# Performance work log

Hardware: AMD Instinct MI355X
Metric: run time of the kernel (lower is better)

Reference implementation:

```python
import jax, jax.numpy as jnp
import numpy as np

D = 1024
H = 16
HD = D // H
LN_EPS = 1e-5
RMS_EPS = 1e-6


def layernorm(x, g, b):
    mu = jnp.mean(x, axis=-1, keepdims=True)
    var = jnp.mean(jnp.square(x - mu), axis=-1, keepdims=True)
    return (x - mu) * jax.lax.rsqrt(var + LN_EPS) * g + b


def rmsnorm(x, w):
    ms = jnp.mean(jnp.square(x), axis=-1, keepdims=True)
    return x * jax.lax.rsqrt(ms + RMS_EPS) * w


def setup_inputs() -> dict:
    key = jax.random.key(0)
    ks = jax.random.split(key, 8)
    s = 0.02
    ones = jnp.ones((D,), jnp.float32)
    zeros = jnp.zeros((D,), jnp.float32)
    return {
        "query_tokens": jax.random.normal(ks[0], (4, 512, D), jnp.float32),
        "point_features": jax.random.normal(ks[1], (4, 4096, D), jnp.float32),
        "ln_q_g": ones, "ln_q_b": zeros,
        "ln_kv_g": ones, "ln_kv_b": zeros,
        "Wq": jax.random.normal(ks[2], (D, D), jnp.float32) * s, "bq": zeros,
        "Wk": jax.random.normal(ks[3], (D, D), jnp.float32) * s, "bk": zeros,
        "Wv": jax.random.normal(ks[4], (D, D), jnp.float32) * s, "bv": zeros,
        "rms_q_w": ones, "rms_k_w": ones,
        "Wo": jax.random.normal(ks[5], (D, D), jnp.float32) * s, "bo": zeros,
        "ln_mlp_g": ones, "ln_mlp_b": zeros,
        "W1": jax.random.normal(ks[6], (D, 4 * D), jnp.float32) * s,
        "b1": jnp.zeros((4 * D,), jnp.float32),
        "W2": jax.random.normal(ks[7], (4 * D, D), jnp.float32) * s,
        "b2": zeros,
    }


def reference(query_tokens, point_features, ln_q_g, ln_q_b, ln_kv_g, ln_kv_b,
              Wq, bq, Wk, bk, Wv, bv, rms_q_w, rms_k_w, Wo, bo,
              ln_mlp_g, ln_mlp_b, W1, b1, W2, b2):
    B, K, _ = query_tokens.shape
    N = point_features.shape[1]
    q_in = layernorm(query_tokens, ln_q_g, ln_q_b)
    kv_in = layernorm(point_features, ln_kv_g, ln_kv_b)
    q = rmsnorm(q_in @ Wq + bq, rms_q_w)          # [B,K,D]
    k = rmsnorm(kv_in @ Wk + bk, rms_k_w)         # [B,N,D]
    v = kv_in @ Wv + bv                            # [B,N,D]
    q = q.reshape(B, K, H, HD)
    k = k.reshape(B, N, H, HD)
    v = v.reshape(B, N, H, HD)
    scores = jnp.einsum('bkhd,bnhd->bhkn', q, k) / jnp.sqrt(jnp.float32(HD))
    attn = jax.nn.softmax(scores, axis=-1)
    ctx = jnp.einsum('bhkn,bnhd->bkhd', attn, v).reshape(B, K, D)
    out = ctx @ Wo + bo + query_tokens
    h = layernorm(out, ln_mlp_g, ln_mlp_b)
    mlp = jax.nn.gelu(h @ W1 + b1, approximate=False) @ W2 + b2
    return out + mlp
```

## Files before the change

kernel.cpp:

```cpp
#include <hip/hip_runtime.h>
#include <math.h>

#define DD   1024
#define NHD  16
#define HDIM 64
#define BB   4
#define QN   512
#define KVN  4096
#define FF   4096

typedef __attribute__((ext_vector_type(8))) short bf16x8;
typedef __attribute__((ext_vector_type(4))) float f32x4;

__device__ __forceinline__ float b2f(ushort u){
  union { unsigned u32; float f; } x; x.u32 = ((unsigned)u)<<16; return x.f;
}
__device__ __forceinline__ ushort f2b(float f){
  unsigned u = __float_as_uint(f);
  unsigned r = (u + 0x7FFFu + ((u>>16)&1u)) >> 16;
  return (ushort)r;
}
__device__ __forceinline__ float ldx(const void* p, size_t i, int isbf){
  return isbf ? b2f(((const ushort*)p)[i]) : ((const float*)p)[i];
}
__device__ __forceinline__ int detect_bf(const void* gref){
  return ((const unsigned*)gref)[0] == 0x3F803F80u;
}

#if defined(__has_builtin)
#if __has_builtin(__builtin_amdgcn_global_load_lds)
#define HAS_GLL 1
#endif
#endif
#ifndef HAS_GLL
#define HAS_GLL 0
#endif
__device__ __forceinline__ void stage16(const ushort* g, ushort* lds_base, int lane){
#if HAS_GLL
  __builtin_amdgcn_global_load_lds(g, lds_base, 16, 0, 0);
#else
  *(uint4*)(lds_base + lane*8) = *(const uint4*)g;
#endif
}

__device__ __forceinline__ void wave_barrier(){
  asm volatile("" ::: "memory");
  __builtin_amdgcn_s_barrier();
  asm volatile("" ::: "memory");
}

__global__ __launch_bounds__(256)
void trans_all(const void* __restrict__ Wq, const void* __restrict__ Wk,
               const void* __restrict__ Wv, const void* __restrict__ Wo,
               const void* __restrict__ W1, const void* __restrict__ W2,
               ushort* __restrict__ WqT, ushort* __restrict__ WkvT,
               ushort* __restrict__ WoT,
               ushort* __restrict__ W1T, ushort* __restrict__ W2T,
               const void* __restrict__ gref)
{
  const int isbf = detect_bf(gref);
  int bid = blockIdx.x;
  const void* src; ushort* dst; int R, C, tid;
  if (bid < 1024){
    int s = bid >> 8; tid = bid & 255; R = 1024; C = 1024;
    src = (s==0) ? Wq : (s==1) ? Wk : (s==2) ? Wv : Wo;
    dst = (s==0) ? WqT : (s==1) ? WkvT : (s==2) ? (WkvT + (size_t)1024*1024) : WoT;
  } else if (bid < 2048){ tid = bid - 1024; src = W1; dst = W1T; R = 1024; C = 4096; }
  else                  { tid = bid - 2048; src = W2; dst = W2T; R = 4096; C = 1024; }
  int ntx = C >> 6;
  int tx = tid % ntx, ty = tid / ntx;
  int r0 = ty*64, c0 = tx*64;

  __shared__ __align__(16) ushort tile[64][72];
  int t = threadIdx.x;
  if (isbf){
    #pragma unroll
    for (int i=0;i<2;i++){
      int idx = t + i*256;
      int r = idx>>3, ch = idx&7;
      #pragma unroll
      for (int j=0;j<8;j++)
        tile[r][ch*8+j] = ((const ushort*)src)[(size_t)(r0+r)*C + c0 + ch*8 + j];
    }
  } else {
    #pragma unroll
    for (int i=0;i<2;i++){
      int idx = t + i*256;
      int r = idx>>3, ch = idx&7;
      const float* s4 = (const float*)src + (size_t)(r0+r)*C + c0 + ch*8;
      float4 f0 = *(const float4*)s4;
      float4 f1 = *(const float4*)(s4+4);
      tile[r][ch*8+0]=f2b(f0.x); tile[r][ch*8+1]=f2b(f0.y);
      tile[r][ch*8+2]=f2b(f0.z); tile[r][ch*8+3]=f2b(f0.w);
      tile[r][ch*8+4]=f2b(f1.x); tile[r][ch*8+5]=f2b(f1.y);
      tile[r][ch*8+6]=f2b(f1.z); tile[r][ch*8+7]=f2b(f1.w);
    }
  }
  __syncthreads();
  #pragma unroll
  for (int i=0;i<2;i++){
    int idx = t + i*256;
    int c = idx>>3, ch = idx&7;
    __align__(16) ushort tmp[8];
    #pragma unroll
    for (int j=0;j<8;j++) tmp[j] = tile[ch*8+j][c];
    *(uint4*)(dst + (size_t)(c0+c)*R + r0 + ch*8) = *(uint4*)tmp;
  }
}

__global__ __launch_bounds__(256)
void ln_all(const void* __restrict__ qtok, const void* __restrict__ pfeat,
            const void* __restrict__ gq, const void* __restrict__ bq,
            const void* __restrict__ gkv, const void* __restrict__ bkv,
            ushort* __restrict__ q_ln, ushort* __restrict__ kv_ln,
            const void* __restrict__ gref)
{
  const int isbf = detect_bf(gref);
  int row = blockIdx.x, t = threadIdx.x;
  const void* src; const void* g; const void* bb; ushort* dst; int r;
  if (row < BB*QN){ src = qtok;  g = gq;  bb = bq;  dst = q_ln;  r = row; }
  else            { src = pfeat; g = gkv; bb = bkv; dst = kv_ln; r = row - BB*QN; }
  int c0 = t*4;
  float v[4];
  if (isbf){
    #pragma unroll
    for (int i=0;i<4;i++) v[i] = b2f(((const ushort*)src)[(size_t)r*DD + c0 + i]);
  } else {
    float4 f = *(const float4*)((const float*)src + (size_t)r*DD + c0);
    v[0]=f.x; v[1]=f.y; v[2]=f.z; v[3]=f.w;
  }
  float s1=0.f, s2=0.f;
  #pragma unroll
  for (int i=0;i<4;i++){ s1 += v[i]; s2 += v[i]*v[i]; }
  #pragma unroll
  for (int off=32; off; off>>=1){ s1 += __shfl_xor(s1,off,64); s2 += __shfl_xor(s2,off,64); }
  __shared__ float r1[4], r2[4];
  int wave = t>>6;
  if ((t&63)==0){ r1[wave]=s1; r2[wave]=s2; }
  __syncthreads();
  s1 = r1[0]+r1[1]+r1[2]+r1[3];
  s2 = r2[0]+r2[1]+r2[2]+r2[3];
  float mu  = s1 * (1.0f/DD);
  float var = s2 * (1.0f/DD) - mu*mu;
  float rs  = rsqrtf(var + 1e-5f);
  union { ushort u[4]; uint2 w; } pk;
  #pragma unroll
  for (int i=0;i<4;i++)
    pk.u[i] = f2b((v[i]-mu)*rs*ldx(g,c0+i,isbf) + ldx(bb,c0+i,isbf));
  *(uint2*)(dst + (size_t)r*DD + c0) = pk.w;
}

__global__ __launch_bounds__(256)
void ln_combine(const float* __restrict__ p0, const float* __restrict__ p1,
                const void* __restrict__ bo, const void* __restrict__ qtok,
                const void* __restrict__ g, const void* __restrict__ bb,
                float* __restrict__ outb, ushort* __restrict__ y,
                const void* __restrict__ gref)
{
  const int isbf = detect_bf(gref);
  int row = blockIdx.x, t = threadIdx.x;
  int c0 = t*4;
  size_t base = (size_t)row*DD + c0;
  float4 a0 = *(const float4*)(p0 + base);
  float4 a1 = *(const float4*)(p1 + base);
  float v[4] = {a0.x+a1.x, a0.y+a1.y, a0.z+a1.z, a0.w+a1.w};
  if (isbf){
    #pragma unroll
    for (int i=0;i<4;i++)
      v[i] += b2f(((const ushort*)qtok)[base+i]) + b2f(((const ushort*)bo)[c0+i]);
  } else {
    float4 q4 = *(const float4*)((const float*)qtok + base);
    v[0] += q4.x + ((const float*)bo)[c0+0];
    v[1] += q4.y + ((const float*)bo)[c0+1];
    v[2] += q4.z + ((const float*)bo)[c0+2];
    v[3] += q4.w + ((const float*)bo)[c0+3];
  }
  float4 ov; ov.x=v[0]; ov.y=v[1]; ov.z=v[2]; ov.w=v[3];
  *(float4*)(outb + base) = ov;

  float s1=0.f, s2=0.f;
  #pragma unroll
  for (int i=0;i<4;i++){ s1 += v[i]; s2 += v[i]*v[i]; }
  #pragma unroll
  for (int off=32; off; off>>=1){ s1 += __shfl_xor(s1,off,64); s2 += __shfl_xor(s2,off,64); }
  __shared__ float r1[4], r2[4];
  int wave = t>>6;
  if ((t&63)==0){ r1[wave]=s1; r2[wave]=s2; }
  __syncthreads();
  s1 = r1[0]+r1[1]+r1[2]+r1[3];
  s2 = r2[0]+r2[1]+r2[2]+r2[3];
  float mu  = s1 * (1.0f/DD);
  float var = s2 * (1.0f/DD) - mu*mu;
  float rs  = rsqrtf(var + 1e-5f);
  union { ushort u[4]; uint2 w; } pk;
  #pragma unroll
  for (int i=0;i<4;i++)
    pk.u[i] = f2b((v[i]-mu)*rs*ldx(g,c0+i,isbf) + ldx(bb,c0+i,isbf));
  *(uint2*)(y + base) = pk.w;
}

__global__ __launch_bounds__(256)
void combine_w2(const float* __restrict__ parts, const void* __restrict__ b2,
                const float* __restrict__ res, void* __restrict__ out,
                const void* __restrict__ gref)
{
  const int isbf = detect_bf(gref);
  size_t i = ((size_t)blockIdx.x*256 + threadIdx.x)*4;
  float4 v = *(const float4*)(parts + i);
  #pragma unroll
  for (int z=1; z<4; z++){
    float4 p = *(const float4*)(parts + (size_t)z*BB*QN*DD + i);
    v.x+=p.x; v.y+=p.y; v.z+=p.z; v.w+=p.w;
  }
  float4 r = *(const float4*)(res + i);
  int col = (int)(i & (DD-1));
  v.x += r.x + ldx(b2,col+0,isbf);
  v.y += r.y + ldx(b2,col+1,isbf);
  v.z += r.z + ldx(b2,col+2,isbf);
  v.w += r.w + ldx(b2,col+3,isbf);
  if (isbf){
    union { ushort u[4]; uint2 w; } pk;
    pk.u[0]=f2b(v.x); pk.u[1]=f2b(v.y); pk.u[2]=f2b(v.z); pk.u[3]=f2b(v.w);
    *(uint2*)((ushort*)out + i) = pk.w;
  } else {
    *(float4*)((float*)out + i) = v;
  }
}

__global__ __launch_bounds__(256)
void rms_all(ushort* __restrict__ qb, const void* __restrict__ wq,
             ushort* __restrict__ kb, const void* __restrict__ wk,
             const void* __restrict__ gref)
{
  const int isbf = detect_bf(gref);
  int row = blockIdx.x, t = threadIdx.x;
  ushort* x; const void* w; int r;
  if (row < BB*QN){ x = qb; w = wq; r = row; }
  else            { x = kb; w = wk; r = row - BB*QN; }
  int c0 = t*4;
  union { ushort u[4]; uint2 w; } in;
  in.w = *(const uint2*)(x + (size_t)r*DD + c0);
  float v[4];
  #pragma unroll
  for (int i=0;i<4;i++) v[i] = b2f(in.u[i]);
  float s2 = 0.f;
  #pragma unroll
  for (int i=0;i<4;i++) s2 += v[i]*v[i];
  #pragma unroll
  for (int off=32; off; off>>=1) s2 += __shfl_xor(s2,off,64);
  __shared__ float r2[4];
  int wave = t>>6;
  if ((t&63)==0) r2[wave]=s2;
  __syncthreads();
  s2 = r2[0]+r2[1]+r2[2]+r2[3];
  float rs = rsqrtf(s2*(1.0f/DD) + 1e-6f);
  union { ushort u[4]; uint2 w; } pk;
  #pragma unroll
  for (int i=0;i<4;i++) pk.u[i] = f2b(v[i]*rs*ldx(w,c0+i,isbf));
  *(uint2*)(x + (size_t)r*DD + c0) = pk.w;
}

template<int ACT_GELU, int OUT_MODE, int RES_MODE>
__global__ __launch_bounds__(256)
void gemm_bt(const ushort* __restrict__ A, const ushort* __restrict__ BT,
             const void* __restrict__ bias,
             const void* __restrict__ res_ext, const float* __restrict__ res_f,
             void* __restrict__ Cout, void* __restrict__ Cout2,
             int M, int N, int Kdim, int Kstride,
             const void* __restrict__ gref)
{
  const int isbf = detect_bf(gref);
  __shared__ __align__(16) ushort As[128*64];
  __shared__ __align__(16) ushort Bs[128*64];
  const int bm = blockIdx.y * 128;
  const int bn = blockIdx.x * 128;
  const int kz = blockIdx.z;
  const int t = threadIdx.x;
  const int wave = t>>6, lane = t&63, quad = lane>>4, l16 = lane&15;
  const int wm = (wave&1)*64, wn = (wave>>1)*64;

  const ushort* ga[4]; const ushort* gb[4];
  #pragma unroll
  for (int j=0;j<4;j++){
    int row = (t>>3) + j*32;
    int g = ((t&7) - row) & 7;
    ga[j] = A  + (size_t)(bm+row)*Kstride + kz*Kdim + g*8;
    gb[j] = BT + (size_t)(bn+row)*Kstride + kz*Kdim + g*8;
  }

  int offA[2][4], offB[2][4];
  #pragma unroll
  for (int kk=0;kk<2;kk++)
    #pragma unroll
    for (int i=0;i<4;i++){
      int ra = wm + i*16 + l16;
      offA[kk][i] = ra*64 + ((quad + kk*4 + ra)&7)*8;
      int rb = wn + i*16 + l16;
      offB[kk][i] = rb*64 + ((quad + kk*4 + rb)&7)*8;
    }

  f32x4 zero = {0.f,0.f,0.f,0.f};
  f32x4 acc[4][4];
  #pragma unroll
  for (int i=0;i<4;i++)
    #pragma unroll
    for (int j=0;j<4;j++) acc[i][j] = zero;

  const int kiters = Kdim >> 6;
  for (int ki = 0; ki < kiters; ki++) {
    #pragma unroll
    for (int j=0;j<4;j++){
      stage16(ga[j], As + (size_t)(j*256 + wave*64)*8, lane);
      stage16(gb[j], Bs + (size_t)(j*256 + wave*64)*8, lane);
      ga[j] += 64; gb[j] += 64;
    }
    __syncthreads();
    #pragma unroll
    for (int kk=0;kk<2;kk++){
      bf16x8 af[4], bfr[4];
      #pragma unroll
      for (int i=0;i<4;i++){
        af[i]  = *(const bf16x8*)(As + offA[kk][i]);
        bfr[i] = *(const bf16x8*)(Bs + offB[kk][i]);
      }
      #pragma unroll
      for (int mt=0;mt<4;mt++)
        #pragma unroll
        for (int nt=0;nt<4;nt++)
          acc[mt][nt] = __builtin_amdgcn_mfma_f32_16x16x32_bf16(af[mt], bfr[nt], acc[mt][nt], 0,0,0);
    }
    __syncthreads();
  }

  if (OUT_MODE == 4){
    float* P = (float*)Cout + (size_t)kz*M*N;
    #pragma unroll
    for (int mt=0;mt<4;mt++){
      #pragma unroll
      for (int r=0;r<4;r++){
        int row = bm + wm + mt*16 + quad*4 + r;
        #pragma unroll
        for (int nt=0;nt<4;nt++){
          int col = bn + wn + nt*16 + l16;
          P[(size_t)row*N + col] = acc[mt][nt][r];
        }
      }
    }
    return;
  }

  if (OUT_MODE == 3){
    if (bn < 1024){
      float bv[4];
      #pragma unroll
      for (int nt=0;nt<4;nt++) bv[nt] = ldx(bias, bn + wn + nt*16 + l16, isbf);
      ushort* kout = (ushort*)Cout;
      #pragma unroll
      for (int mt=0;mt<4;mt++){
        #pragma unroll
        for (int r=0;r<4;r++){
          int row = bm + wm + mt*16 + quad*4 + r;
          #pragma unroll
          for (int nt=0;nt<4;nt++){
            int col = bn + wn + nt*16 + l16;
            kout[(size_t)row*1024 + col] = f2b(acc[mt][nt][r] + bv[nt]);
          }
        }
      }
    } else {
      float bv[4];
      #pragma unroll
      for (int nt=0;nt<4;nt++) bv[nt] = ldx(res_ext, bn-1024 + wn + nt*16 + l16, isbf);
      ushort* Vt = (ushort*)Cout2;
      #pragma unroll
      for (int mt=0;mt<4;mt++){
        int row0 = bm + wm + mt*16 + quad*4;
        int b = row0 >> 12, tok = row0 & (KVN-1);
        #pragma unroll
        for (int nt=0;nt<4;nt++){
          int cl = bn-1024 + wn + nt*16 + l16;
          union { ushort u[4]; uint2 w; } pk;
          #pragma unroll
          for (int r=0;r<4;r++) pk.u[r] = f2b(acc[mt][nt][r] + bv[nt]);
          size_t o = ((size_t)((b*NHD + (cl>>6))*HDIM + (cl&63)))*KVN + tok;
          *(uint2*)(Vt + o) = pk.w;
        }
      }
    }
    return;
  }

  float bv[4];
  #pragma unroll
  for (int nt=0;nt<4;nt++) bv[nt] = ldx(bias, bn + wn + nt*16 + l16, isbf);
  #pragma unroll
  for (int mt=0;mt<4;mt++){
    #pragma unroll
    for (int r=0;r<4;r++){
      int row = bm + wm + mt*16 + quad*4 + r;
      #pragma unroll
      for (int nt=0;nt<4;nt++){
        int col = bn + wn + nt*16 + l16;
        float v = acc[mt][nt][r] + bv[nt];
        if (ACT_GELU) v = 0.5f*v*(1.0f + erff(v*0.70710678118f));
        size_t oi = (size_t)row*N + col;
        if (RES_MODE==1) v += ldx(res_ext, oi, isbf);
        if (RES_MODE==2) v += res_f[oi];
        if (OUT_MODE==0)      ((ushort*)Cout)[oi] = f2b(v);
        else if (OUT_MODE==1) ((float*)Cout)[oi]  = v;
        else { if (isbf) ((ushort*)Cout)[oi] = f2b(v); else ((float*)Cout)[oi] = v; }
      }
    }
  }
}

#define G_HB  32768
#define G_RA0 0
#define G_RA1 8192
#define G_RB0 16384
#define G_RB1 24576

#define G_STAGE(src, R, tile) do{ \
  ushort* _d = ldsb + (((tile)&1)*G_HB + (R) + wave*1024); \
  stage16(src[0] + ((tile)<<6), _d,       lane); \
  stage16(src[1] + ((tile)<<6), _d + 512, lane); \
}while(0)

#define G_LDA(dst, base) \
  _Pragma("unroll") for (int kk=0;kk<2;kk++) \
  _Pragma("unroll") for (int m=0;m<4;m++) \
    dst[kk][m] = *(const bf16x8*)((base) + offA[kk][m]);

#define G_LDB(dst, base) \
  _Pragma("unroll") for (int kk=0;kk<2;kk++) \
  _Pragma("unroll") for (int n=0;n<2;n++) \
    dst[kk][n] = *(const bf16x8*)((base) + offB[kk][n]);

#define G_MM16(ar, br, MO, NO) \
  _Pragma("unroll") for (int kk=0;kk<2;kk++) \
  _Pragma("unroll") for (int m=0;m<4;m++) \
  _Pragma("unroll") for (int n=0;n<2;n++) \
    acc[m+(MO)][n+(NO)] = __builtin_amdgcn_mfma_f32_16x16x32_bf16(ar[kk][m], br[kk][n], acc[m+(MO)][n+(NO)], 0,0,0);

#define G_SYNC() do{ wave_barrier(); \
  asm volatile("s_waitcnt lgkmcnt(0)" ::: "memory"); \
  __builtin_amdgcn_sched_barrier(0); \
  __builtin_amdgcn_s_setprio(1); }while(0)

#define G_END() do{ __builtin_amdgcn_s_setprio(0); wave_barrier(); }while(0)

__global__ __launch_bounds__(512, 2)
void gemm256_kv(const ushort* __restrict__ A, const ushort* __restrict__ BT,
                const void* __restrict__ biasK, const void* __restrict__ biasV,
                ushort* __restrict__ Kout, ushort* __restrict__ Vt,
                int Kdim, const void* __restrict__ gref)
{
  const int isbf = detect_bf(gref);
  __shared__ __align__(16) ushort ldsb[65536];
  const int bm = blockIdx.y * 256;
  const int bn = blockIdx.x * 256;
  const int t = threadIdx.x;
  const int wave = t>>6, lane = t&63, quad = lane>>4, l16 = lane&15;
  const int wg = wave>>2, wn = wave&3;

  const ushort *sA0[2], *sA1[2], *sB0[2], *sB1[2];
  #pragma unroll
  for (int jj=0;jj<2;jj++){
    int r = (wave*2 + jj)*8 + (lane>>3);
    int g = ((lane&7) - r) & 7;
    int grA0 = r + (r & 64);
    int gc0  = (r & 31) + ((r >> 5) << 6);
    sA0[jj] = A  + (size_t)(bm + grA0     )*Kdim + g*8;
    sA1[jj] = A  + (size_t)(bm + grA0 + 64)*Kdim + g*8;
    sB0[jj] = BT + (size_t)(bn + gc0      )*Kdim + g*8;
    sB1[jj] = BT + (size_t)(bn + gc0 + 32 )*Kdim + g*8;
  }

  int offA[2][4], offB[2][2];
  #pragma unroll
  for (int kk=0;kk<2;kk++){
    int slot = ((kk*4 + quad + l16) & 7) * 8;
    #pragma unroll
    for (int m=0;m<4;m++) offA[kk][m] = (wg*64 + m*16 + l16)*64 + slot;
    #pragma unroll
    for (int n=0;n<2;n++) offB[kk][n] = (wn*32 + n*16 + l16)*64 + slot;
  }

  f32x4 zero = {0.f,0.f,0.f,0.f};
  f32x4 acc[8][4];
  #pragma unroll
  for (int i=0;i<8;i++)
    #pragma unroll
    for (int j=0;j<4;j++) acc[i][j] = zero;

  G_STAGE(sA0, G_RA0, 0);
  G_STAGE(sB0, G_RB0, 0);
  G_STAGE(sB1, G_RB1, 0);
  G_STAGE(sA1, G_RA1, 0);
  G_STAGE(sA0, G_RA0, 1);
  G_STAGE(sB1, G_RB1, 1);
  G_STAGE(sA1, G_RA1, 1);
  asm volatile("s_waitcnt vmcnt(6)" ::: "memory");
  wave_barrier();

  const int niter = Kdim >> 7;
  const ushort* L0 = ldsb;
  const ushort* L1 = ldsb + G_HB;
  bf16x8 a[2][4], b[2][2], b1[2][2];

  for (int i = 0; i < niter; ++i) {
    const bool st = (i + 1 < niter);
    G_LDA(a, L0 + G_RA0); G_LDB(b, L0 + G_RB0);
    G_STAGE(sB0, G_RB0, 2*i+1);
    G_SYNC(); G_MM16(a, b, 0, 0); G_END();
    G_LDB(b1, L0 + G_RB1);
    if (st) G_STAGE(sA0, G_RA0, 2*i+2);
    G_SYNC(); G_MM16(a, b1, 0, 2); G_END();
    G_LDA(a, L0 + G_RA1);
    if (st) G_STAGE(sB1, G_RB1, 2*i+2);
    G_SYNC(); G_MM16(a, b1, 4, 2); G_END();
    if (st) G_STAGE(sA1, G_RA1, 2*i+2);
    G_SYNC(); G_MM16(a, b, 4, 0);
    __builtin_amdgcn_s_setprio(0);
    if (st) { asm volatile("s_waitcnt vmcnt(6)" ::: "memory"); }
    else    { asm volatile("s_waitcnt vmcnt(0)" ::: "memory"); }
    wave_barrier();
    G_LDA(a, L1 + G_RA0); G_LDB(b, L1 + G_RB0);
    if (st) G_STAGE(sB0, G_RB0, 2*i+2);
    G_SYNC(); G_MM16(a, b, 0, 0); G_END();
    G_LDB(b1, L1 + G_RB1);
    if (st) G_STAGE(sA0, G_RA0, 2*i+3);
    G_SYNC(); G_MM16(a, b1, 0, 2); G_END();
    G_LDA(a, L1 + G_RA1);
    if (st) G_STAGE(sB1, G_RB1, 2*i+3);
    G_SYNC(); G_MM16(a, b1, 4, 2); G_END();
    if (st) G_STAGE(sA1, G_RA1, 2*i+3);
    G_SYNC(); G_MM16(a, b, 4, 0);
    __builtin_amdgcn_s_setprio(0);
    if (st) { asm volatile("s_waitcnt vmcnt(6)" ::: "memory"); }
    wave_barrier();
  }

  if (bn < 1024){
    float bvv[4];
    #pragma unroll
    for (int nt=0;nt<4;nt++) bvv[nt] = ldx(biasK, bn + wn*64 + nt*16 + l16, isbf);
    #pragma unroll
    for (int mt=0;mt<8;mt++){
      #pragma unroll
      for (int r=0;r<4;r++){
        int row = bm + wg*128 + mt*16 + quad*4 + r;
        #pragma unroll
        for (int nt=0;nt<4;nt++){
          int col = bn + wn*64 + nt*16 + l16;
          Kout[(size_t)row*1024 + col] = f2b(acc[mt][nt][r] + bvv[nt]);
        }
      }
    }
  } else {
    float bvv[4];
    #pragma unroll
    for (int nt=0;nt<4;nt++) bvv[nt] = ldx(biasV, bn - 1024 + wn*64 + nt*16 + l16, isbf);
    #pragma unroll
    for (int mt=0;mt<8;mt++){
      int row0 = bm + wg*128 + mt*16 + quad*4;
      int bi = row0 >> 12, tok = row0 & (KVN-1);
      #pragma unroll
      for (int nt=0;nt<4;nt++){
        int cl = bn - 1024 + wn*64 + nt*16 + l16;
        union { ushort u[4]; uint2 w2; } pk;
        #pragma unroll
        for (int r=0;r<4;r++) pk.u[r] = f2b(acc[mt][nt][r] + bvv[nt]);
        size_t o = ((size_t)((bi*NHD + (cl>>6))*HDIM + (cl&63)))*KVN + tok;
        *(uint2*)(Vt + o) = pk.w2;
      }
    }
  }
}

__global__ __launch_bounds__(256, 3)
void flash_attn3(const ushort* __restrict__ Q, const ushort* __restrict__ K,
                 const ushort* __restrict__ Vt, float* __restrict__ Op,
                 float* __restrict__ ML)
{
  __shared__ __align__(16) ushort Ks[128*72];
  __shared__ __align__(16) ushort Vs[64*136];
  __shared__ __align__(16) ushort Ps[4][16*136];
  const int bh = blockIdx.x, qt = blockIdx.y, hf = blockIdx.z;
  const int b = bh>>4, h = bh&15;
  const int t = threadIdx.x, wave = t>>6, lane = t&63, quad = lane>>4, l16 = lane&15;
  ushort* Pz = Ps[wave];

  const float QS = 0.125f * 1.4426950408889634f;
  bf16x8 qf[2][2];
  #pragma unroll
  for (int mt=0;mt<2;mt++){
    const ushort* qb = Q + (size_t)(b*QN + qt*128 + wave*32 + mt*16 + l16)*DD + h*HDIM;
    bf16x8 r0 = *(const bf16x8*)(qb + quad*8);
    bf16x8 r1 = *(const bf16x8*)(qb + 32 + quad*8);
    #pragma unroll
    for (int j=0;j<8;j++){
      qf[mt][0][j] = (short)f2b(b2f((ushort)r0[j]) * QS);
      qf[mt][1][j] = (short)f2b(b2f((ushort)r1[j]) * QS);
    }
  }

  f32x4 zero = {0.f,0.f,0.f,0.f};
  f32x4 o[2][4];
  #pragma unroll
  for (int mt=0;mt<2;mt++)
    #pragma unroll
    for (int nt=0;nt<4;nt++) o[mt][nt] = zero;
  float lp[2][4] = {{0.f,0.f,0.f,0.f},{0.f,0.f,0.f,0.f}};

  const ushort* kgb = K  + (size_t)(b*KVN + hf*1024)*DD + h*HDIM;
  const ushort* vtb = Vt + ((size_t)bh*HDIM)*KVN + hf*1024;
  const int kcs = t&7;

  for (int kv0 = 0; kv0 < 1024; kv0 += 128) {
    #pragma unroll
    for (int j=0;j<4;j++){
      int kr = (t>>3) + j*32;
      *(uint4*)(Ks + kr*72 + kcs*8) =
        *(const uint4*)(kgb + (size_t)(kv0+kr)*DD + kcs*8);
    }
    #pragma unroll
    for (int j=0;j<4;j++){
      int p = t + j*256; int vr = p>>4, vc = p&15;
      uint4 d = *(const uint4*)(vtb + (size_t)vr*KVN + kv0 + vc*8);
      ushort* pv = (ushort*)&d;
      ushort* vbp = Vs + vr*136 + (vc&1)*64 + (vc>>1);
      #pragma unroll
      for (int jj=0;jj<8;jj++) vbp[jj*8] = pv[jj];
    }
    __syncthreads();

    f32x4 pb[2][8];
    #pragma unroll
    for (int nt=0;nt<8;nt++){
      const ushort* kb = Ks + (nt*16+l16)*72 + quad*8;
      bf16x8 kf0 = *(const bf16x8*)kb;
      bf16x8 kf1 = *(const bf16x8*)(kb + 32);
      #pragma unroll
      for (int mt=0;mt<2;mt++){
        f32x4 a = __builtin_amdgcn_mfma_f32_16x16x32_bf16(qf[mt][0], kf0, zero, 0,0,0);
        a = __builtin_amdgcn_mfma_f32_16x16x32_bf16(qf[mt][1], kf1, a, 0,0,0);
        #pragma unroll
        for (int r=0;r<4;r++) a[r] = __builtin_amdgcn_exp2f(fminf(a[r], 88.f));
        pb[mt][nt] = a;
      }
    }
    #pragma unroll
    for (int mt=0;mt<2;mt++){
      #pragma unroll
      for (int r=0;r<4;r++){
        float ls = 0.f;
        bf16x8 pk;
        #pragma unroll
        for (int nt=0;nt<8;nt++){
          ls += pb[mt][nt][r];
          pk[nt] = (short)(__float_as_uint(pb[mt][nt][r]) >> 16);
        }
        lp[mt][r] += ls;
        *(bf16x8*)(Pz + (quad*4+r)*136 + l16*8) = pk;
      }
      #pragma unroll
      for (int kc=0;kc<4;kc++){
        bf16x8 pa = *(const bf16x8*)(Pz + l16*136 + kc*32 + quad*8);
        pb[mt][kc] = *(f32x4*)&pa;
      }
    }
    #pragma unroll
    for (int nt=0;nt<4;nt++){
      const ushort* vbr = Vs + (nt*16+l16)*136;
      #pragma unroll
      for (int kc=0;kc<4;kc++){
        bf16x8 vf = *(const bf16x8*)(vbr + kc*32 + quad*8);
        o[0][nt] = __builtin_amdgcn_mfma_f32_16x16x32_bf16(*(bf16x8*)&pb[0][kc], vf, o[0][nt], 0,0,0);
        o[1][nt] = __builtin_amdgcn_mfma_f32_16x16x32_bf16(*(bf16x8*)&pb[1][kc], vf, o[1][nt], 0,0,0);
      }
    }
    __syncthreads();
  }

  const int slot = hf*256 + bh*4 + qt;
  float* Ob = Op + (size_t)slot*128*64;
  #pragma unroll
  for (int mt=0;mt<2;mt++)
    #pragma unroll
    for (int nt=0;nt<4;nt++)
      #pragma unroll
      for (int r=0;r<4;r++)
        Ob[(wave*32 + mt*16 + quad*4 + r)*64 + nt*16 + l16] = o[mt][nt][r];
  #pragma unroll
  for (int mt=0;mt<2;mt++)
    #pragma unroll
    for (int r=0;r<4;r++){
      float v = lp[mt][r];
      #pragma unroll
      for (int off=1; off<16; off<<=1) v += __shfl_xor(v, off, 64);
      if (l16 == 0)
        ML[(size_t)slot*128 + wave*32 + mt*16 + quad*4 + r] = v;
    }
}

__global__ __launch_bounds__(256)
void flash_combine4(const float* __restrict__ Op, const float* __restrict__ ML,
                    ushort* __restrict__ Ctx)
{
  const int bq = blockIdx.x;
  const int bh = bq>>2, qt = bq&3;
  const int b = bh>>4, h = bh&15;
  const int t = threadIdx.x;
  const int row = t>>1, hd0 = (t&1)*32;
  float l = 0.f;
  #pragma unroll
  for (int i=0;i<4;i++) l += ML[(size_t)(i*256 + bq)*128 + row];
  float inv = 1.0f / l;
  float4 a[8];
  #pragma unroll
  for (int c=0;c<8;c++){ a[c].x=0.f; a[c].y=0.f; a[c].z=0.f; a[c].w=0.f; }
  #pragma unroll
  for (int i=0;i<4;i++){
    const float* s = Op + ((size_t)(i*256 + bq)*128 + row)*64 + hd0;
    #pragma unroll
    for (int c=0;c<8;c++){
      float4 v = *(const float4*)(s + c*4);
      a[c].x += v.x; a[c].y += v.y; a[c].z += v.z; a[c].w += v.w;
    }
  }
  ushort* dst = Ctx + (size_t)(b*QN + qt*128 + row)*DD + h*HDIM + hd0;
  #pragma unroll
  for (int c=0;c<8;c++){
    union { ushort u[4]; uint2 w; } pk;
    pk.u[0] = f2b(a[c].x*inv); pk.u[1] = f2b(a[c].y*inv);
    pk.u[2] = f2b(a[c].z*inv); pk.u[3] = f2b(a[c].w*inv);
    *(uint2*)(dst + c*4) = pk.w;
  }
}

extern "C" void kernel_launch(void* const* d_in, const int* in_sizes, int n_in,
                              void* d_out, int out_size, void* d_ws, size_t ws_size,
                              hipStream_t stream)
{
  const void* qtok    = d_in[0];
  const void* pfeat   = d_in[1];
  const void* ln_q_g  = d_in[2];
  const void* ln_q_b  = d_in[3];
  const void* ln_kv_g = d_in[4];
  const void* ln_kv_b = d_in[5];
  const void* Wq      = d_in[6];
  const void* bq      = d_in[7];
  const void* Wk      = d_in[8];
  const void* bk      = d_in[9];
  const void* Wv      = d_in[10];
  const void* bv      = d_in[11];
  const void* rms_q_w = d_in[12];
  const void* rms_k_w = d_in[13];
  const void* Wo      = d_in[14];
  const void* bo      = d_in[15];
  const void* ln_mlp_g= d_in[16];
  const void* ln_mlp_b= d_in[17];
  const void* W1      = d_in[18];
  const void* b1      = d_in[19];
  const void* W2      = d_in[20];
  const void* b2      = d_in[21];
  const void* gref    = ln_q_g;

  char* w = (char*)d_ws;
  auto take = [&](size_t bytes)->char*{ char* p = w; w += (bytes + 255) & ~(size_t)255; return p; };
  ushort* WqT  = (ushort*)take((size_t)DD*DD*2);
  ushort* WkvT = (ushort*)take((size_t)2*DD*DD*2);
  ushort* WoT  = (ushort*)take((size_t)DD*DD*2);
  ushort* W1T  = (ushort*)take((size_t)DD*FF*2);
  ushort* W2T  = (ushort*)take((size_t)FF*DD*2);
  ushort* kv_ln= (ushort*)take((size_t)BB*KVN*DD*2);
  ushort* q_ln = (ushort*)take((size_t)BB*QN*DD*2);
  ushort* kbuf = (ushort*)take((size_t)BB*KVN*DD*2);
  ushort* qbuf = (ushort*)take((size_t)BB*QN*DD*2);
  ushort* Vt   = (ushort*)take((size_t)BB*KVN*DD*2);
  ushort* ctx  = WqT;
  float*  outb = (float*)kbuf;
  ushort* mlp1 = kv_ln;
  float*  Op   = (float*)kv_ln;
  float*  ML   = (float*)q_ln;
  float*  o_parts  = (float*)kv_ln;
  float*  w2_parts = (float*)Vt;
  ushort* h_ln = q_ln;

  trans_all<<<3072,256,0,stream>>>(Wq,Wk,Wv,Wo,W1,W2, WqT,WkvT,WoT,W1T,W2T, gref);
  ln_all<<<BB*QN + BB*KVN,256,0,stream>>>(qtok,pfeat, ln_q_g,ln_q_b, ln_kv_g,ln_kv_b,
                                          q_ln, kv_ln, gref);
  gemm_bt<0,0,0><<<dim3(8,16), 256,0,stream>>>(q_ln,  WqT, bq, nullptr,nullptr,
                                               qbuf, nullptr, BB*QN, DD, DD, DD, gref);
  gemm256_kv<<<dim3(2*DD/256, BB*KVN/256), 512, 0, stream>>>(kv_ln, WkvT, bk, bv,
                                                             kbuf, Vt, DD, gref);
  rms_all<<<BB*QN + BB*KVN,256,0,stream>>>(qbuf, rms_q_w, kbuf, rms_k_w, gref);
  flash_attn3<<<dim3(64,4,4),256,0,stream>>>(qbuf, kbuf, Vt, Op, ML);
  flash_combine4<<<256,256,0,stream>>>(Op, ML, ctx);
  gemm_bt<0,4,0><<<dim3(8,16,2),256,0,stream>>>(ctx, WoT, nullptr, nullptr,nullptr,
                                                o_parts, nullptr, BB*QN, DD, DD/2, DD, gref);
  ln_combine<<<BB*QN,256,0,stream>>>(o_parts, o_parts + (size_t)BB*QN*DD,
                                     bo, qtok, ln_mlp_g, ln_mlp_b, outb, h_ln, gref);
  gemm_bt<1,0,0><<<dim3(32,16),256,0,stream>>>(h_ln, W1T, b1, nullptr,nullptr,
                                               mlp1, nullptr, BB*QN, FF, DD, DD, gref);
  gemm_bt<0,4,0><<<dim3(8,16,4),256,0,stream>>>(mlp1, W2T, nullptr, nullptr,nullptr,
                                                w2_parts, nullptr, BB*QN, DD, FF/4, FF, gref);
  combine_w2<<<BB*QN*DD/1024,256,0,stream>>>(w2_parts, b2, outb, d_out, gref);
}
```

Baseline: 521.8 us.

## Fuse Q projection into KV 256-tile GEMM and use 256-tile split-K for W2

Generalizes the 256x256 KV GEMM kernel into a templated gemm256. Mode 0 computes the Q projection in the same launch as K/V, using a swizzled block index, which removes a separate launch and fills idle CUs. Mode 1 runs the W2 GEMM with the larger tile and 8-way split-K, writing partials to three scattered workspace regions that combine_w2 now sums (8 partials instead of 4). This trades extra partial-sum memory traffic and workspace aliasing risk for better tile efficiency and occupancy.

```diff
diff --git a/kernel.cpp b/kernel.cpp
--- a/kernel.cpp
+++ b/kernel.cpp
@@ -200,16 +200,28 @@
 }
 
 __global__ __launch_bounds__(256)
-void combine_w2(const float* __restrict__ parts, const void* __restrict__ b2,
+void combine_w2(const float* __restrict__ P0, const float* __restrict__ P1,
+                const float* __restrict__ P2, const void* __restrict__ b2,
                 const float* __restrict__ res, void* __restrict__ out,
                 const void* __restrict__ gref)
 {
   const int isbf = detect_bf(gref);
+  const size_t PSZ = (size_t)BB*QN*DD;
   size_t i = ((size_t)blockIdx.x*256 + threadIdx.x)*4;
-  float4 v = *(const float4*)(parts + i);
+  float4 v = *(const float4*)(P0 + i);
   #pragma unroll
   for (int z=1; z<4; z++){
-    float4 p = *(const float4*)(parts + (size_t)z*BB*QN*DD + i);
+    float4 p = *(const float4*)(P0 + (size_t)z*PSZ + i);
+    v.x+=p.x; v.y+=p.y; v.z+=p.z; v.w+=p.w;
+  }
+  #pragma unroll
+  for (int z=0; z<2; z++){
+    float4 p = *(const float4*)(P1 + (size_t)z*PSZ + i);
+    v.x+=p.x; v.y+=p.y; v.z+=p.z; v.w+=p.w;
+  }
+  #pragma unroll
+  for (int z=0; z<2; z++){
+    float4 p = *(const float4*)(P2 + (size_t)z*PSZ + i);
     v.x+=p.x; v.y+=p.y; v.z+=p.z; v.w+=p.w;
   }
   float4 r = *(const float4*)(res + i);
@@ -349,47 +361,6 @@
     return;
   }
 
-  if (OUT_MODE == 3){
-    if (bn < 1024){
-      float bv[4];
-      #pragma unroll
-      for (int nt=0;nt<4;nt++) bv[nt] = ldx(bias, bn + wn + nt*16 + l16, isbf);
-      ushort* kout = (ushort*)Cout;
-      #pragma unroll
-      for (int mt=0;mt<4;mt++){
-        #pragma unroll
-        for (int r=0;r<4;r++){
-          int row = bm + wm + mt*16 + quad*4 + r;
-          #pragma unroll
-          for (int nt=0;nt<4;nt++){
-            int col = bn + wn + nt*16 + l16;
-            kout[(size_t)row*1024 + col] = f2b(acc[mt][nt][r] + bv[nt]);
-          }
-        }
-      }
-    } else {
-      float bv[4];
-      #pragma unroll
-      for (int nt=0;nt<4;nt++) bv[nt] = ldx(res_ext, bn-1024 + wn + nt*16 + l16, isbf);
-      ushort* Vt = (ushort*)Cout2;
-      #pragma unroll
-      for (int mt=0;mt<4;mt++){
-        int row0 = bm + wm + mt*16 + quad*4;
-        int b = row0 >> 12, tok = row0 & (KVN-1);
-        #pragma unroll
-        for (int nt=0;nt<4;nt++){
-          int cl = bn-1024 + wn + nt*16 + l16;
-          union { ushort u[4]; uint2 w; } pk;
-          #pragma unroll
-          for (int r=0;r<4;r++) pk.u[r] = f2b(acc[mt][nt][r] + bv[nt]);
-          size_t o = ((size_t)((b*NHD + (cl>>6))*HDIM + (cl&63)))*KVN + tok;
-          *(uint2*)(Vt + o) = pk.w;
-        }
-      }
-    }
-    return;
-  }
-
   float bv[4];
   #pragma unroll
   for (int nt=0;nt<4;nt++) bv[nt] = ldx(bias, bn + wn + nt*16 + l16, isbf);
@@ -449,16 +420,37 @@
 
 #define G_END() do{ __builtin_amdgcn_s_setprio(0); wave_barrier(); }while(0)
 
+template<int MODE>
 __global__ __launch_bounds__(512, 2)
-void gemm256_kv(const ushort* __restrict__ A, const ushort* __restrict__ BT,
-                const void* __restrict__ biasK, const void* __restrict__ biasV,
-                ushort* __restrict__ Kout, ushort* __restrict__ Vt,
-                int Kdim, const void* __restrict__ gref)
+void gemm256(const ushort* __restrict__ A, const ushort* __restrict__ Aq,
+             const ushort* __restrict__ BT, const ushort* __restrict__ BTq,
+             const void* __restrict__ biasK, const void* __restrict__ biasV,
+             const void* __restrict__ biasQ,
+             ushort* __restrict__ Kout, ushort* __restrict__ Vt,
+             ushort* __restrict__ Qout,
+             float* __restrict__ P0, float* __restrict__ P1,
+             float* __restrict__ P2,
+             int Kdim, int Kstride,
+             const void* __restrict__ gref)
 {
   const int isbf = detect_bf(gref);
   __shared__ __align__(16) ushort ldsb[65536];
-  const int bm = blockIdx.y * 256;
-  const int bn = blockIdx.x * 256;
+  const int nb = blockIdx.x;
+  int bx, by, kz = 0; bool qmode = false;
+  if (MODE == 0){
+    int k = nb & 7, j = nb >> 3;
+    if (j < 64){ int kvid = 64*k + j; bx = kvid & 7; by = kvid >> 3; }
+    else { int qid = 8*k + (j - 64); bx = qid & 7; by = qid >> 3; qmode = true;
+           if (bx >= 4) return; }
+  } else {
+    int wsw = (nb & 7)*32 + (nb >> 3);
+    bx = wsw & 3; by = (wsw >> 2) & 7; kz = wsw >> 5;
+  }
+  const ushort* Ab = (MODE==0 && qmode) ? Aq : A;
+  const ushort* Bb = (MODE==0 && qmode) ? BTq : BT;
+  const int bmrow = by*256;
+  const int bn = bx*256;
+  const int koff = (MODE==1) ? kz*Kdim : 0;
   const int t = threadIdx.x;
   const int wave = t>>6, lane = t&63, quad = lane>>4, l16 = lane&15;
   const int wg = wave>>2, wn = wave&3;
@@ -470,10 +462,10 @@
     int g = ((lane&7) - r) & 7;
     int grA0 = r + (r & 64);
     int gc0  = (r & 31) + ((r >> 5) << 6);
-    sA0[jj] = A  + (size_t)(bm + grA0     )*Kdim + g*8;
-    sA1[jj] = A  + (size_t)(bm + grA0 + 64)*Kdim + g*8;
-    sB0[jj] = BT + (size_t)(bn + gc0      )*Kdim + g*8;
-    sB1[jj] = BT + (size_t)(bn + gc0 + 32 )*Kdim + g*8;
+    sA0[jj] = Ab + (size_t)(bmrow + grA0     )*Kstride + koff + g*8;
+    sA1[jj] = Ab + (size_t)(bmrow + grA0 + 64)*Kstride + koff + g*8;
+    sB0[jj] = Bb + (size_t)(bn + gc0      )*Kstride + koff + g*8;
+    sB1[jj] = Bb + (size_t)(bn + gc0 + 32 )*Kstride + koff + g*8;
   }
 
   int offA[2][4], offB[2][2];
@@ -541,15 +533,50 @@
     wave_barrier();
   }
 
-  if (bn < 1024){
+  if (MODE == 1){
+    const size_t PSZ = (size_t)BB*QN*DD;
+    float* P = (kz < 4) ? P0 + (size_t)kz*PSZ
+             : (kz < 6) ? P1 + (size_t)(kz-4)*PSZ
+                        : P2 + (size_t)(kz-6)*PSZ;
+    #pragma unroll
+    for (int mt=0;mt<8;mt++){
+      #pragma unroll
+      for (int r=0;r<4;r++){
+        int row = bmrow + wg*128 + mt*16 + quad*4 + r;
+        #pragma unroll
+        for (int nt=0;nt<4;nt++){
+          int col = bn + wn*64 + nt*16 + l16;
+          P[(size_t)row*1024 + col] = acc[mt][nt][r];
+        }
+      }
+    }
+    return;
+  }
+  if (qmode){
     float bvv[4];
     #pragma unroll
+    for (int nt=0;nt<4;nt++) bvv[nt] = ldx(biasQ, bn + wn*64 + nt*16 + l16, isbf);
+    #pragma unroll
+    for (int mt=0;mt<8;mt++){
+      #pragma unroll
+      for (int r=0;r<4;r++){
+        int row = bmrow + wg*128 + mt*16 + quad*4 + r;
+        #pragma unroll
+        for (int nt=0;nt<4;nt++){
+          int col = bn + wn*64 + nt*16 + l16;
+          Qout[(size_t)row*1024 + col] = f2b(acc[mt][nt][r] + bvv[nt]);
+        }
+      }
+    }
+  } else if (bn < 1024){
+    float bvv[4];
+    #pragma unroll
     for (int nt=0;nt<4;nt++) bvv[nt] = ldx(biasK, bn + wn*64 + nt*16 + l16, isbf);
     #pragma unroll
     for (int mt=0;mt<8;mt++){
       #pragma unroll
       for (int r=0;r<4;r++){
-        int row = bm + wg*128 + mt*16 + quad*4 + r;
+        int row = bmrow + wg*128 + mt*16 + quad*4 + r;
         #pragma unroll
         for (int nt=0;nt<4;nt++){
           int col = bn + wn*64 + nt*16 + l16;
@@ -563,7 +590,7 @@
     for (int nt=0;nt<4;nt++) bvv[nt] = ldx(biasV, bn - 1024 + wn*64 + nt*16 + l16, isbf);
     #pragma unroll
     for (int mt=0;mt<8;mt++){
-      int row0 = bm + wg*128 + mt*16 + quad*4;
+      int row0 = bmrow + wg*128 + mt*16 + quad*4;
       int bi = row0 >> 12, tok = row0 & (KVN-1);
       #pragma unroll
       for (int nt=0;nt<4;nt++){
@@ -785,16 +812,17 @@
   float*  Op   = (float*)kv_ln;
   float*  ML   = (float*)q_ln;
   float*  o_parts  = (float*)kv_ln;
-  float*  w2_parts = (float*)Vt;
   ushort* h_ln = q_ln;
+  float*  w2p0 = (float*)Vt;
+  float*  w2p1 = (float*)(kv_ln + (size_t)8*1024*1024);
+  float*  w2p2 = (float*)d_ws;
 
   trans_all<<<3072,256,0,stream>>>(Wq,Wk,Wv,Wo,W1,W2, WqT,WkvT,WoT,W1T,W2T, gref);
   ln_all<<<BB*QN + BB*KVN,256,0,stream>>>(qtok,pfeat, ln_q_g,ln_q_b, ln_kv_g,ln_kv_b,
                                           q_ln, kv_ln, gref);
-  gemm_bt<0,0,0><<<dim3(8,16), 256,0,stream>>>(q_ln,  WqT, bq, nullptr,nullptr,
-                                               qbuf, nullptr, BB*QN, DD, DD, DD, gref);
-  gemm256_kv<<<dim3(2*DD/256, BB*KVN/256), 512, 0, stream>>>(kv_ln, WkvT, bk, bv,
-                                                             kbuf, Vt, DD, gref);
+  gemm256<0><<<576, 512, 0, stream>>>(kv_ln, q_ln, WkvT, WqT, bk, bv, bq,
+                                      kbuf, Vt, qbuf, nullptr, nullptr, nullptr,
+                                      DD, DD, gref);
   rms_all<<<BB*QN + BB*KVN,256,0,stream>>>(qbuf, rms_q_w, kbuf, rms_k_w, gref);
   flash_attn3<<<dim3(64,4,4),256,0,stream>>>(qbuf, kbuf, Vt, Op, ML);
   flash_combine4<<<256,256,0,stream>>>(Op, ML, ctx);
@@ -804,7 +832,9 @@
                                      bo, qtok, ln_mlp_g, ln_mlp_b, outb, h_ln, gref);
   gemm_bt<1,0,0><<<dim3(32,16),256,0,stream>>>(h_ln, W1T, b1, nullptr,nullptr,
                                                mlp1, nullptr, BB*QN, FF, DD, DD, gref);
-  gemm_bt<0,4,0><<<dim3(8,16,4),256,0,stream>>>(mlp1, W2T, nullptr, nullptr,nullptr,
-                                                w2_parts, nullptr, BB*QN, DD, FF/4, FF, gref);
-  combine_w2<<<BB*QN*DD/1024,256,0,stream>>>(w2_parts, b2, outb, d_out, gref);
-}
+  gemm256<1><<<256, 512, 0, stream>>>(mlp1, nullptr, W2T, nullptr,
+                                      nullptr, nullptr, nullptr,
+                                      nullptr, nullptr, nullptr,
+                                      w2p0, w2p1, w2p2, FF/8, FF, gref);
+  combine_w2<<<BB*QN*DD/1024,256,0,stream>>>(w2p0, w2p1, w2p2, b2, outb, d_out, gref);
+}
```

Result: no change. 515.5 us (-1.2%).
